# Optimization experiments

Hardware: AMD Instinct MI355X
Metric: run time of the kernel (lower is better)

The kernel has to match this reference:

```python
import jax, jax.numpy as jnp
import numpy as np

B = 4096      # batch rows
T = 8192      # hop_length (time steps per call)
N = 256       # n_taps = len(b)


def setup_inputs() -> dict:
    key = jax.random.key(0)
    kx, kb, kz = jax.random.split(key, 3)
    x = jax.random.normal(kx, (B, T), dtype=jnp.float32)
    # FIR coefficients (nn.Parameter b in the torch module)
    b = jax.random.normal(kb, (N,), dtype=jnp.float32) / N
    # 'zeros_init' is an nn.Parameter initialized to zeros but learned; use small
    # nonzero values so its contribution to the math is exercised.
    zeros_init = jax.random.normal(kz, (N, T), dtype=jnp.float32) * 0.01
    return {"x": x, "b": b, "zeros_init": zeros_init}


def reference(x, b, zeros_init):
    # Torch module semantics: per-step the recurrence keeps a length-N buffer
    #   buff_t = [x_t, buff_{t-1}[0:N-1]]            (shift-in, drop oldest)
    #   y_t    = sum_k b[k] * buff_t[k] = sum_k b[k] * x_{t-k}
    # with initial buffer buff_{-1} = x @ zeros_init.T, i.e. zi[:, j] plays the
    # role of x_{-1-j} for j = 0..N-2 (zi[:, N-1] is shifted out before use).
    # This is exactly a causal FIR / depthwise 1-D convolution, which we fuse
    # into a single valid convolution over an extended signal.
    n = b.shape[0]
    zi = x @ zeros_init.T                       # [B, N] initial buffer
    hist = jnp.flip(zi[:, : n - 1], axis=-1)    # [B, N-1]: x_{-(N-1)} .. x_{-1}
    x_ext = jnp.concatenate([hist, x], axis=-1)  # [B, T + N - 1]
    # lax conv is cross-correlation: out[t] = sum_j k[j] * in[t+j];
    # we need out[t] = sum_k b[k] * x_ext[t + N-1 - k]  ->  kernel = flip(b).
    y = jax.lax.conv_general_dilated(
        x_ext[:, None, :],                      # [B, 1, T+N-1]  (NCW)
        jnp.flip(b)[None, None, :],             # [1, 1, N]      (OIW)
        window_strides=(1,),
        padding="VALID",
    )
    return y[:, 0, :]                           # [B, T]
```

## Files before the change

### kernel.cpp

```cpp
#include <hip/hip_runtime.h>
#include <hip/hip_bf16.h>

#define B_ROWS 4096
#define T_LEN  8192
#define N_TAPS 256

typedef __attribute__((ext_vector_type(8))) short short8;
typedef __attribute__((ext_vector_type(4))) short short4v;
typedef __attribute__((ext_vector_type(4))) float f32x4;

__device__ inline ushort f2bf(float f) {
    __hip_bfloat16 h = __float2bfloat16(f);
    union { __hip_bfloat16 h; ushort u; } c;
    c.h = h;
    return c.u;
}

__global__ __launch_bounds__(256) void fir_cast_z(const float* __restrict__ z,
                                                  ushort* __restrict__ zbf) {
    const int idx = (blockIdx.x * 256 + threadIdx.x) * 8;
    float4 a = *(const float4*)&z[idx];
    float4 b = *(const float4*)&z[idx + 4];
    short8 o;
    o[0] = (short)f2bf(a.x); o[1] = (short)f2bf(a.y);
    o[2] = (short)f2bf(a.z); o[3] = (short)f2bf(a.w);
    o[4] = (short)f2bf(b.x); o[5] = (short)f2bf(b.y);
    o[6] = (short)f2bf(b.z); o[7] = (short)f2bf(b.w);
    *(short8*)&zbf[idx] = o;
}

__global__ void fir_build_wtab(const float* __restrict__ b,
                               ushort* __restrict__ wtab) {
    const int a = blockIdx.x;
    const int lane = threadIdx.x;
    const int l15 = lane & 15, lg = lane >> 4;
    short8 o;
    #pragma unroll
    for (int j = 0; j < 8; ++j) {
        const int bi = 16 * a - 32 + l15 - lg * 8 - j;
        const float v = (bi >= 0 && bi < N_TAPS) ? b[bi] : 0.f;
        o[j] = (short)f2bf(v);
    }
    *(short8*)&wtab[(a * 64 + lane) * 8] = o;
}

#define MT 64
#define GBK 64

__global__ __launch_bounds__(256, 2) void fir_zi_gemm(
        const float* __restrict__ x,
        const ushort* __restrict__ zbf,
        float* __restrict__ part,
        int kslices) {
    __shared__ ushort As[MT * GBK];
    __shared__ ushort Bs[N_TAPS * GBK];
    const int i0 = blockIdx.x * MT;
    const int ks = blockIdx.y;
    const int klen = T_LEN / kslices;
    const int kbase = ks * klen;
    const int tid = threadIdx.x;
    const int wn = tid >> 6;
    const int lane = tid & 63;
    const int l15 = lane & 15, lg = lane >> 4;

    const int a_r = tid >> 4;
    const int a_c4 = (tid & 15) * 4;
    const int b_r0 = tid >> 3;
    const int b_c8 = (tid & 7) * 8;

    f32x4 acc[4][4];
    #pragma unroll
    for (int mi = 0; mi < 4; ++mi)
        #pragma unroll
        for (int ni = 0; ni < 4; ++ni) acc[mi][ni] = (f32x4){0.f, 0.f, 0.f, 0.f};

    const int nt = klen / GBK;

    float4 apf[4];
    short8 bpf[8];

    auto loadT = [&](int kc) {
        #pragma unroll
        for (int q = 0; q < 4; ++q) {
            const int r = a_r;
            apf[q] = *(const float4*)&x[(size_t)(i0 + a_r + q * 16) * T_LEN
                                        + kbase + kc + a_c4];
            (void)r;
        }
        #pragma unroll
        for (int q = 0; q < 8; ++q) {
            bpf[q] = *(const short8*)&zbf[(size_t)(b_r0 + q * 32) * T_LEN
                                          + kbase + kc + b_c8];
        }
    };
    auto storeT = [&]() {
        #pragma unroll
        for (int q = 0; q < 4; ++q) {
            const int r = a_r + q * 16;
            short4v o;
            o[0] = (short)f2bf(apf[q].x); o[1] = (short)f2bf(apf[q].y);
            o[2] = (short)f2bf(apf[q].z); o[3] = (short)f2bf(apf[q].w);
            const int boff = r * 128 + ((a_c4 * 2) ^ ((r & 7) << 4));
            *(short4v*)((char*)As + boff) = o;
        }
        #pragma unroll
        for (int q = 0; q < 8; ++q) {
            const int r = b_r0 + q * 32;
            const int boff = r * 128 + ((b_c8 * 2) ^ ((r & 7) << 4));
            *(short8*)((char*)Bs + boff) = bpf[q];
        }
    };

    loadT(0);
    for (int t = 0; t < nt; ++t) {
        __syncthreads();
        storeT();
        if (t + 1 < nt) loadT((t + 1) * GBK);
        __syncthreads();
        #pragma unroll
        for (int ksb = 0; ksb < 2; ++ksb) {
            short8 af[4], bfr[4];
            const int cb = (lg * 8 + ksb * 32) * 2;
            #pragma unroll
            for (int mi = 0; mi < 4; ++mi) {
                const int row = mi * 16 + l15;
                af[mi] = *(const short8*)((const char*)As + row * 128
                                          + (cb ^ ((row & 7) << 4)));
            }
            #pragma unroll
            for (int ni = 0; ni < 4; ++ni) {
                const int row = wn * 64 + ni * 16 + l15;
                bfr[ni] = *(const short8*)((const char*)Bs + row * 128
                                           + (cb ^ ((row & 7) << 4)));
            }
            #pragma unroll
            for (int mi = 0; mi < 4; ++mi)
                #pragma unroll
                for (int ni = 0; ni < 4; ++ni)
                    acc[mi][ni] = __builtin_amdgcn_mfma_f32_16x16x32_bf16(
                        af[mi], bfr[ni], acc[mi][ni], 0, 0, 0);
        }
    }

    #pragma unroll
    for (int mi = 0; mi < 4; ++mi) {
        #pragma unroll
        for (int ni = 0; ni < 4; ++ni) {
            const int gn = wn * 64 + ni * 16 + l15;
            #pragma unroll
            for (int rg = 0; rg < 4; ++rg) {
                const int gm = i0 + mi * 16 + lg * 4 + rg;
                part[((size_t)ks * B_ROWS + gm) * N_TAPS + gn] = acc[mi][ni][rg];
            }
        }
    }
}

__global__ __launch_bounds__(256) void fir_zi_reduce(const float* __restrict__ part,
                                                     float* __restrict__ zi,
                                                     int kslices) {
    const int idx = blockIdx.x * 256 + threadIdx.x;
    const int total = B_ROWS * N_TAPS / 4;
    if (idx >= total) return;
    float4 s = ((const float4*)part)[idx];
    for (int q = 1; q < kslices; ++q) {
        float4 v = ((const float4*)part)[(size_t)q * total + idx];
        s.x += v.x; s.y += v.y; s.z += v.z; s.w += v.w;
    }
    ((float4*)zi)[idx] = s;
}

#define VBM 16
#define VBT 1024
#define VWIN 1280
#define VSTR 2560

__global__ __launch_bounds__(256, 2) void fir_conv_mfma(
        const float* __restrict__ x,
        const ushort* __restrict__ wtab,
        const float* __restrict__ zi,
        float* __restrict__ y) {
    __shared__ ushort xe[VBM * VSTR / 2];
    const int t0 = blockIdx.x * VBT;
    const int i0 = blockIdx.y * VBM;
    const int tid = threadIdx.x;
    const int lane = tid & 63, wid = tid >> 6;
    const int l15 = lane & 15, lg = lane >> 4;

    short8 wf[18];
    #pragma unroll
    for (int a = 0; a < 18; ++a)
        wf[a] = *(const short8*)&wtab[((a + 2) * 64 + lane) * 8];

    #pragma unroll
    for (int it = 0; it < 8; ++it) {
        const int e = tid + it * 256;
        const int r = e >> 7;
        const int c8 = e & 127;
        const int g = t0 + c8 * 8;
        float4 v0 = *(const float4*)&x[(size_t)(i0 + r) * T_LEN + g];
        float4 v1 = *(const float4*)&x[(size_t)(i0 + r) * T_LEN + g + 4];
        short8 o;
        o[0] = (short)f2bf(v0.x); o[1] = (short)f2bf(v0.y);
        o[2] = (short)f2bf(v0.z); o[3] = (short)f2bf(v0.w);
        o[4] = (short)f2bf(v1.x); o[5] = (short)f2bf(v1.y);
        o[6] = (short)f2bf(v1.z); o[7] = (short)f2bf(v1.w);
        const int off = (512 + c8 * 16) ^ ((r & 7) << 4);
        *(short8*)((char*)xe + r * VSTR + off) = o;
    }
    #pragma unroll
    for (int it = 0; it < 2; ++it) {
        const int e = tid + it * 256;
        const int r = e >> 5;
        const int c8 = e & 31;
        const int g = t0 - 256 + c8 * 8;
        short8 o;
        if (g >= 0) {
            float4 v0 = *(const float4*)&x[(size_t)(i0 + r) * T_LEN + g];
            float4 v1 = *(const float4*)&x[(size_t)(i0 + r) * T_LEN + g + 4];
            o[0] = (short)f2bf(v0.x); o[1] = (short)f2bf(v0.y);
            o[2] = (short)f2bf(v0.z); o[3] = (short)f2bf(v0.w);
            o[4] = (short)f2bf(v1.x); o[5] = (short)f2bf(v1.y);
            o[6] = (short)f2bf(v1.z); o[7] = (short)f2bf(v1.w);
        } else {
            #pragma unroll
            for (int jj = 0; jj < 8; ++jj)
                o[jj] = (short)f2bf(zi[(size_t)(i0 + r) * N_TAPS + (-1 - g - jj)]);
        }
        const int off = (c8 * 16) ^ ((r & 7) << 4);
        *(short8*)((char*)xe + r * VSTR + off) = o;
    }
    __syncthreads();

    f32x4 acc[4][4];
    #pragma unroll
    for (int c4 = 0; c4 < 4; ++c4)
        #pragma unroll
        for (int n = 0; n < 4; ++n) acc[c4][n] = (f32x4){0.f, 0.f, 0.f, 0.f};

    const int chunk0 = wid * 4;
    #pragma unroll
    for (int ui = 0; ui < 10; ++ui) {
        #pragma unroll
        for (int c4 = 0; c4 < 4; ++c4) {
            const int colw = (chunk0 + c4) * 64 + ui * 32 + lg * 8;
            const int off = (colw * 2) ^ ((l15 & 7) << 4);
            short8 af = *(const short8*)((const char*)xe + l15 * VSTR + off);
            #pragma unroll
            for (int ncol = 0; ncol < 4; ++ncol) {
                const int a = ncol + 18 - 2 * ui;
                if (a >= 2 && a <= 19)
                    acc[c4][ncol] = __builtin_amdgcn_mfma_f32_16x16x32_bf16(
                        af, wf[a - 2], acc[c4][ncol], 0, 0, 0);
            }
        }
    }

    #pragma unroll
    for (int c4 = 0; c4 < 4; ++c4) {
        #pragma unroll
        for (int ncol = 0; ncol < 4; ++ncol) {
            const size_t tcol = (size_t)t0 + (chunk0 + c4) * 64 + ncol * 16 + l15;
            #pragma unroll
            for (int rg = 0; rg < 4; ++rg) {
                y[(size_t)(i0 + lg * 4 + rg) * T_LEN + tcol] = acc[c4][ncol][rg];
            }
        }
    }
}

extern "C" void kernel_launch(void* const* d_in, const int* in_sizes, int n_in,
                              void* d_out, int out_size, void* d_ws, size_t ws_size,
                              hipStream_t stream) {
    const float* x  = (const float*)d_in[0];
    const float* b  = (const float*)d_in[1];
    const float* z  = (const float*)d_in[2];
    float* y = (float*)d_out;

    char* ws = (char*)d_ws;
    float*  zi   = (float*)ws;
    ushort* zbf  = (ushort*)(ws + (4u << 20));
    ushort* wtab = (ushort*)(ws + (8u << 20));
    float*  part = (float*)(ws + (8u << 20) + (64u << 10));

    int kslices = 8;
    while (kslices > 1 &&
           (size_t)(8u << 20) + (64u << 10) + (size_t)kslices * (4u << 20) > ws_size)
        kslices >>= 1;

    fir_build_wtab<<<22, 64, 0, stream>>>(b, wtab);
    fir_cast_z<<<N_TAPS * T_LEN / (256 * 8), 256, 0, stream>>>(z, zbf);

    dim3 ggrid(B_ROWS / MT, kslices);
    fir_zi_gemm<<<ggrid, 256, 0, stream>>>(x, zbf, part, kslices);

    fir_zi_reduce<<<B_ROWS * N_TAPS / 4 / 256, 256, 0, stream>>>(part, zi, kslices);

    dim3 cgrid(T_LEN / VBT, B_ROWS / VBM);
    fir_conv_mfma<<<cgrid, 256, 0, stream>>>(x, wtab, zi, y);
}
```

Before: 105.6 us.

## Load GEMM tiles directly into LDS via global_load_lds, convert A at fragment read

The zi GEMM now uses the buffer_load-to-LDS path (global_load_lds, 16 bytes) for both the x tile and the bf16 z tile, skipping the register staging round-trip. The x tile stays fp32 in shared memory with an XOR swizzle applied on the global-address side, and each wave converts it to bf16 as it builds MFMA fragments. The register-prefetch software pipeline is removed, so loads and MFMAs no longer overlap within a block. Overlap now depends on running two blocks per CU, and the A tile in LDS doubles in size.

```diff
diff --git a/kernel.cpp b/kernel.cpp
--- a/kernel.cpp
+++ b/kernel.cpp
@@ -14,6 +14,12 @@
     union { __hip_bfloat16 h; ushort u; } c;
     c.h = h;
     return c.u;
+}
+
+typedef __attribute__((address_space(1))) const void g_void;
+typedef __attribute__((address_space(3))) void s_void;
+__device__ inline void gload16(const void* g, void* s) {
+    __builtin_amdgcn_global_load_lds((g_void*)g, (s_void*)s, 16, 0, 0);
 }
 
 __global__ __launch_bounds__(256) void fir_cast_z(const float* __restrict__ z,
@@ -52,21 +58,21 @@
         const ushort* __restrict__ zbf,
         float* __restrict__ part,
         int kslices) {
-    __shared__ ushort As[MT * GBK];
+    __shared__ float  Asf[MT * GBK];
     __shared__ ushort Bs[N_TAPS * GBK];
     const int i0 = blockIdx.x * MT;
     const int ks = blockIdx.y;
     const int klen = T_LEN / kslices;
     const int kbase = ks * klen;
     const int tid = threadIdx.x;
-    const int wn = tid >> 6;
+    const int wid = tid >> 6;
     const int lane = tid & 63;
     const int l15 = lane & 15, lg = lane >> 4;
 
-    const int a_r = tid >> 4;
-    const int a_c4 = (tid & 15) * 4;
-    const int b_r0 = tid >> 3;
-    const int b_c8 = (tid & 7) * 8;
+    const int a_rl = lane >> 4;
+    const int a_lc = lane & 15;
+    const int b_rl = lane >> 3;
+    const int b_lc = lane & 7;
 
     f32x4 acc[4][4];
     #pragma unroll
@@ -76,62 +82,50 @@
 
     const int nt = klen / GBK;
 
-    float4 apf[4];
-    short8 bpf[8];
-
-    auto loadT = [&](int kc) {
+    for (int t = 0; t < nt; ++t) {
+        const int kc = kbase + t * GBK;
         #pragma unroll
         for (int q = 0; q < 4; ++q) {
-            const int r = a_r;
-            apf[q] = *(const float4*)&x[(size_t)(i0 + a_r + q * 16) * T_LEN
-                                        + kbase + kc + a_c4];
-            (void)r;
+            const int seg = wid * 4 + q;
+            const int row = seg * 4 + a_rl;
+            const int gc  = a_lc ^ (row & 7);
+            gload16(&x[(size_t)(i0 + row) * T_LEN + kc + gc * 4],
+                    (char*)Asf + seg * 1024);
         }
         #pragma unroll
         for (int q = 0; q < 8; ++q) {
-            bpf[q] = *(const short8*)&zbf[(size_t)(b_r0 + q * 32) * T_LEN
-                                          + kbase + kc + b_c8];
-        }
-    };
-    auto storeT = [&]() {
-        #pragma unroll
-        for (int q = 0; q < 4; ++q) {
-            const int r = a_r + q * 16;
-            short4v o;
-            o[0] = (short)f2bf(apf[q].x); o[1] = (short)f2bf(apf[q].y);
-            o[2] = (short)f2bf(apf[q].z); o[3] = (short)f2bf(apf[q].w);
-            const int boff = r * 128 + ((a_c4 * 2) ^ ((r & 7) << 4));
-            *(short4v*)((char*)As + boff) = o;
-        }
-        #pragma unroll
-        for (int q = 0; q < 8; ++q) {
-            const int r = b_r0 + q * 32;
-            const int boff = r * 128 + ((b_c8 * 2) ^ ((r & 7) << 4));
-            *(short8*)((char*)Bs + boff) = bpf[q];
-        }
-    };
-
-    loadT(0);
-    for (int t = 0; t < nt; ++t) {
+            const int seg = wid * 8 + q;
+            const int row = seg * 8 + b_rl;
+            const int gc  = b_lc ^ (row & 7);
+            gload16(&zbf[(size_t)row * T_LEN + kc + gc * 8],
+                    (char*)Bs + seg * 1024);
+        }
         __syncthreads();
-        storeT();
-        if (t + 1 < nt) loadT((t + 1) * GBK);
-        __syncthreads();
+
         #pragma unroll
         for (int ksb = 0; ksb < 2; ++ksb) {
             short8 af[4], bfr[4];
-            const int cb = (lg * 8 + ksb * 32) * 2;
             #pragma unroll
             for (int mi = 0; mi < 4; ++mi) {
                 const int row = mi * 16 + l15;
-                af[mi] = *(const short8*)((const char*)As + row * 128
-                                          + (cb ^ ((row & 7) << 4)));
+                const int c0 = lg * 2 + ksb * 8;
+                const f32x4 v0 = *(const f32x4*)((const char*)Asf + row * 256
+                                                 + ((c0 ^ (row & 7)) * 16));
+                const f32x4 v1 = *(const f32x4*)((const char*)Asf + row * 256
+                                                 + (((c0 + 1) ^ (row & 7)) * 16));
+                short8 f;
+                f[0] = (short)f2bf(v0[0]); f[1] = (short)f2bf(v0[1]);
+                f[2] = (short)f2bf(v0[2]); f[3] = (short)f2bf(v0[3]);
+                f[4] = (short)f2bf(v1[0]); f[5] = (short)f2bf(v1[1]);
+                f[6] = (short)f2bf(v1[2]); f[7] = (short)f2bf(v1[3]);
+                af[mi] = f;
             }
             #pragma unroll
             for (int ni = 0; ni < 4; ++ni) {
-                const int row = wn * 64 + ni * 16 + l15;
+                const int row = wid * 64 + ni * 16 + l15;
+                const int c = lg + ksb * 4;
                 bfr[ni] = *(const short8*)((const char*)Bs + row * 128
-                                           + (cb ^ ((row & 7) << 4)));
+                                           + ((c ^ (row & 7)) * 16));
             }
             #pragma unroll
             for (int mi = 0; mi < 4; ++mi)
@@ -140,13 +134,14 @@
                     acc[mi][ni] = __builtin_amdgcn_mfma_f32_16x16x32_bf16(
                         af[mi], bfr[ni], acc[mi][ni], 0, 0, 0);
         }
+        __syncthreads();
     }
 
     #pragma unroll
     for (int mi = 0; mi < 4; ++mi) {
         #pragma unroll
         for (int ni = 0; ni < 4; ++ni) {
-            const int gn = wn * 64 + ni * 16 + l15;
+            const int gn = wid * 64 + ni * 16 + l15;
             #pragma unroll
             for (int rg = 0; rg < 4; ++rg) {
                 const int gm = i0 + mi * 16 + lg * 4 + rg;
```

Result: slower. 109.0 us (+3.2%).
